# Kernel optimization log

Hardware: AMD Instinct MI355X
Metric: run time of the kernel (lower is better)

The kernel has to match this reference:

```python
import jax, jax.numpy as jnp
import numpy as np

S, B, V, E, H = 512, 16, 32003, 512, 512
HH = H // 2  # per-direction encoder hidden (bidirectional LSTM)


def _lstm(x, Wih, Whh, b, hsz):
    # x: (T, B, in); Wih: (4h, in); Whh: (4h, h); b: (4h,)  (PyTorch i,f,g,o gate order)
    xW = jnp.einsum('tbi,gi->tbg', x, Wih) + b  # precompute input projections
    h0 = jnp.zeros((x.shape[1], hsz), x.dtype)

    def step(carry, xt):
        h, c = carry
        g = xt + h @ Whh.T
        i, f, gg, o = jnp.split(g, 4, axis=-1)
        c = jax.nn.sigmoid(f) * c + jax.nn.sigmoid(i) * jnp.tanh(gg)
        h = jax.nn.sigmoid(o) * jnp.tanh(c)
        return (h, c), h

    _, hs = jax.lax.scan(step, (h0, h0), xW)
    return hs  # (T, B, hsz)


def setup_inputs() -> dict:
    key = jax.random.key(0)
    k = jax.random.split(key, 16)
    sc = 0.08
    return {
        'numeric': jax.random.randint(k[0], (S, B), 0, V, dtype=jnp.int32),
        'numeric_noised': jax.random.randint(k[1], (S, B), 0, V, dtype=jnp.int32),
        'emb': jax.random.normal(k[2], (V, E), jnp.float32) * sc,
        'enc_Wih_f': jax.random.normal(k[3], (4 * HH, E), jnp.float32) * sc,
        'enc_Whh_f': jax.random.normal(k[4], (4 * HH, HH), jnp.float32) * sc,
        'enc_b_f': jnp.zeros((4 * HH,), jnp.float32),
        'enc_Wih_b': jax.random.normal(k[5], (4 * HH, E), jnp.float32) * sc,
        'enc_Whh_b': jax.random.normal(k[6], (4 * HH, HH), jnp.float32) * sc,
        'enc_b_b': jnp.zeros((4 * HH,), jnp.float32),
        'dec_Wih': jax.random.normal(k[7], (4 * H, E), jnp.float32) * sc,
        'dec_Whh': jax.random.normal(k[8], (4 * H, H), jnp.float32) * sc,
        'dec_b': jnp.zeros((4 * H,), jnp.float32),
        'attn_W': jax.random.normal(k[9], (H, H), jnp.float32) * sc,
        'mlp_W': jax.random.normal(k[10], (H, 2 * H), jnp.float32) * sc,
        'mlp_b': jnp.zeros((H,), jnp.float32),
        'out_W': jax.random.normal(k[11], (V, H), jnp.float32) * sc,
        'out_b': jnp.zeros((V,), jnp.float32),
    }


def reference(numeric, numeric_noised, emb, enc_Wih_f, enc_Whh_f, enc_b_f,
              enc_Wih_b, enc_Whh_b, enc_b_b, dec_Wih, dec_Whh, dec_b,
              attn_W, mlp_W, mlp_b, out_W, out_b):
    zero = jnp.zeros((1, B), numeric.dtype)  # zeroBeginning (<SOS>=0)
    num = jnp.concatenate([zero, numeric], 0)            # (S+1, B)
    noised = jnp.concatenate([zero, numeric_noised], 0)  # (S+1, B)
    inp_t, tgt = num[:-1], num[1:]
    embedded = emb[inp_t]        # (S, B, E)
    emb_noised = emb[noised]     # (S+1, B, E)

    # BiLSTM encoder (hidden H/2 per direction)
    ef = _lstm(emb_noised, enc_Wih_f, enc_Whh_f, enc_b_f, HH)
    eb = _lstm(emb_noised[::-1], enc_Wih_b, enc_Whh_b, enc_b_b, HH)[::-1]
    enc = jnp.concatenate([ef, eb], -1)                  # (S+1, B, H)

    # LSTM decoder (teacher forced)
    dec = _lstm(embedded, dec_Wih, dec_Whh, dec_b, H)    # (S, B, H)

    # attention: scores over encoder positions s, softmax on dim s
    proj = jnp.einsum('sbh,kh->sbk', enc, attn_W)        # attention_proj (no bias)
    scores = jnp.einsum('sbh,tbh->bst', proj, dec)       # (B, S+1, S)
    attn = jax.nn.softmax(scores, axis=1)
    # context: equivalent of (enc.unsqueeze(2)*attn.unsqueeze(3)).sum(0).transpose(0,1)
    ctx = jnp.einsum('sbh,bst->tbh', enc, attn)          # (S, B, H)

    full = jnp.concatenate([dec, ctx], -1)               # (S, B, 2H)
    hid = jax.nn.relu(jnp.einsum('tbf,hf->tbh', full, mlp_W) + mlp_b)
    logits = jnp.einsum('tbh,vh->tbv', hid, out_W) + out_b
    logp = jax.nn.log_softmax(logits, -1)

    # NLLLoss with ignore_index=0, mean over non-ignored tokens
    nll = -jnp.take_along_axis(logp, tgt[..., None].astype(jnp.int32), axis=-1)[..., 0]
    mask = (tgt != 0).astype(logp.dtype)
    return (nll * mask).sum() / mask.sum()
```

## Files before the change

kernel.cpp:

```cpp
#include <hip/hip_runtime.h>
#include <stdint.h>
#include <stddef.h>


typedef __attribute__((ext_vector_type(8))) short  sx8;
typedef __attribute__((ext_vector_type(8))) __bf16 bfx8;
typedef __attribute__((ext_vector_type(4))) float  fx4;

#define NCHUNK 251

__device__ __forceinline__ float bf2f(short h) {
  unsigned u = ((unsigned)(unsigned short)h) << 16;
  return __builtin_bit_cast(float, u);
}
__device__ __forceinline__ short f2bf(float f) {
  unsigned u = __builtin_bit_cast(unsigned, f);
  u = (u + 0x7fffu + ((u >> 16) & 1u)) >> 16;
  return (short)u;
}
__device__ __forceinline__ fx4 mfma_bf16(sx8 a, sx8 b, fx4 c) {
  return __builtin_amdgcn_mfma_f32_16x16x32_bf16(
      __builtin_bit_cast(bfx8, a), __builtin_bit_cast(bfx8, b), c, 0, 0, 0);
}
__device__ __forceinline__ float sigm(float x) { return 1.f / (1.f + __expf(-x)); }
__device__ __forceinline__ float tanh_f(float x) { return 2.f / (1.f + __expf(-2.f * x)) - 1.f; }

__global__ void k_f32_to_bf16(const float* __restrict__ src, short* __restrict__ dst, long n) {
  long i = (long)blockIdx.x * 256 + threadIdx.x;
  long stride = (long)gridDim.x * 256;
  for (; i < n; i += stride) dst[i] = f2bf(src[i]);
}

__global__ void k_embed(const float* __restrict__ emb, const int* __restrict__ idx,
                        short* __restrict__ dst, int rows) {
  long i = (long)blockIdx.x * 256 + threadIdx.x;
  if (i >= (long)rows * 512) return;
  int r = (int)(i >> 9), c = (int)(i & 511);
  int tok = (r < 16) ? 0 : idx[r - 16];
  dst[i] = f2bf(emb[(size_t)tok * 512 + c]);
}

#define BM 128
#define BN 128
#define BK 32
__global__ __launch_bounds__(256) void k_gemm_bt(
    const short* __restrict__ A, long lda, long sA,
    const short* __restrict__ B, long ldb, long sB,
    short* __restrict__ Cb, float* __restrict__ Cf, long ldc, long sC,
    const float* __restrict__ bias, int relu,
    int M, int N, int K) {
  __shared__ short As[BM * BK];
  __shared__ short Bs[BN * BK];
  const int bz = blockIdx.z;
  const short* Ab = A + (size_t)bz * sA;
  const short* Bb = B + (size_t)bz * sB;
  const int m0 = blockIdx.x * BM, n0 = blockIdx.y * BN;
  const int tid = threadIdx.x;
  const int lane = tid & 63, wave = tid >> 6;
  const int wr = wave >> 1, wc = wave & 1;
  const int q = lane >> 4, l15 = lane & 15;
  const int sr = tid >> 2;
  const int sc = (tid & 3) * 8;

  fx4 acc[4][4] = {};

  for (int k0 = 0; k0 < K; k0 += BK) {
    __syncthreads();
    *(sx8*)&As[ sr       * BK + sc] = *(const sx8*)(Ab + (size_t)(m0 + sr)      * lda + k0 + sc);
    *(sx8*)&As[(sr + 64) * BK + sc] = *(const sx8*)(Ab + (size_t)(m0 + sr + 64) * lda + k0 + sc);
    *(sx8*)&Bs[ sr       * BK + sc] = *(const sx8*)(Bb + (size_t)(n0 + sr)      * ldb + k0 + sc);
    *(sx8*)&Bs[(sr + 64) * BK + sc] = *(const sx8*)(Bb + (size_t)(n0 + sr + 64) * ldb + k0 + sc);
    __syncthreads();
    sx8 af[4], bf[4];
#pragma unroll
    for (int i = 0; i < 4; i++) af[i] = *(const sx8*)&As[(wr * 64 + i * 16 + l15) * BK + q * 8];
#pragma unroll
    for (int j = 0; j < 4; j++) bf[j] = *(const sx8*)&Bs[(wc * 64 + j * 16 + l15) * BK + q * 8];
#pragma unroll
    for (int i = 0; i < 4; i++)
#pragma unroll
      for (int j = 0; j < 4; j++) acc[i][j] = mfma_bf16(af[i], bf[j], acc[i][j]);
  }

#pragma unroll
  for (int i = 0; i < 4; i++) {
    int row0 = m0 + wr * 64 + i * 16 + q * 4;
#pragma unroll
    for (int j = 0; j < 4; j++) {
      int col = n0 + wc * 64 + j * 16 + l15;
      if (col >= N) continue;
      float bv = bias ? bias[col] : 0.f;
#pragma unroll
      for (int r = 0; r < 4; r++) {
        int row = row0 + r;
        if (row >= M) continue;
        float v = acc[i][j][r] + bv;
        if (relu) v = fmaxf(v, 0.f);
        size_t o = (size_t)bz * sC + (size_t)row * ldc + col;
        if (Cb) Cb[o] = f2bf(v);
        else    Cf[o] = v;
      }
    }
  }
}

__global__ __launch_bounds__(256) void k_gemm_lse(
    const short* __restrict__ A, const short* __restrict__ B,
    const float* __restrict__ bias,
    float* __restrict__ mp, float* __restrict__ sp,
    int N, int K) {
  __shared__ short As[BM * BK];
  __shared__ short Bs[BN * BK];
  __shared__ float redm[2][2][64];
  __shared__ float reds[2][2][64];
  const int m0 = blockIdx.x * BM, n0 = blockIdx.y * BN;
  const int tid = threadIdx.x;
  const int lane = tid & 63, wave = tid >> 6;
  const int wr = wave >> 1, wc = wave & 1;
  const int q = lane >> 4, l15 = lane & 15;
  const int sr = tid >> 2, sc = (tid & 3) * 8;

  fx4 acc[4][4] = {};
  for (int k0 = 0; k0 < K; k0 += BK) {
    __syncthreads();
    *(sx8*)&As[ sr       * BK + sc] = *(const sx8*)(A + (size_t)(m0 + sr)      * K + k0 + sc);
    *(sx8*)&As[(sr + 64) * BK + sc] = *(const sx8*)(A + (size_t)(m0 + sr + 64) * K + k0 + sc);
    *(sx8*)&Bs[ sr       * BK + sc] = *(const sx8*)(B + (size_t)(n0 + sr)      * K + k0 + sc);
    *(sx8*)&Bs[(sr + 64) * BK + sc] = *(const sx8*)(B + (size_t)(n0 + sr + 64) * K + k0 + sc);
    __syncthreads();
    sx8 af[4], bf[4];
#pragma unroll
    for (int i = 0; i < 4; i++) af[i] = *(const sx8*)&As[(wr * 64 + i * 16 + l15) * BK + q * 8];
#pragma unroll
    for (int j = 0; j < 4; j++) bf[j] = *(const sx8*)&Bs[(wc * 64 + j * 16 + l15) * BK + q * 8];
#pragma unroll
    for (int i = 0; i < 4; i++)
#pragma unroll
      for (int j = 0; j < 4; j++) acc[i][j] = mfma_bf16(af[i], bf[j], acc[i][j]);
  }

#pragma unroll
  for (int i = 0; i < 4; i++) {
#pragma unroll
    for (int r = 0; r < 4; r++) {
      float vj[4], mx = -1e30f;
#pragma unroll
      for (int j = 0; j < 4; j++) {
        int col = n0 + wc * 64 + j * 16 + l15;
        float v = (col < N) ? (acc[i][j][r] + bias[col]) : -1e30f;
        vj[j] = v;
        mx = fmaxf(mx, v);
      }
#pragma unroll
      for (int off = 1; off < 16; off <<= 1) mx = fmaxf(mx, __shfl_xor(mx, off, 64));
      float s = 0.f;
#pragma unroll
      for (int j = 0; j < 4; j++) s += __expf(vj[j] - mx);
#pragma unroll
      for (int off = 1; off < 16; off <<= 1) s += __shfl_xor(s, off, 64);
      if (l15 == 0) {
        int rl = i * 16 + q * 4 + r;
        redm[wr][wc][rl] = mx;
        reds[wr][wc][rl] = s;
      }
    }
  }
  __syncthreads();
  if (tid < 128) {
    int wrr = tid >> 6, rl = tid & 63;
    float ma = redm[wrr][0][rl], mb = redm[wrr][1][rl];
    float M2 = fmaxf(ma, mb);
    float S2 = reds[wrr][0][rl] * __expf(ma - M2) + reds[wrr][1][rl] * __expf(mb - M2);
    int grow = m0 + wrr * 64 + rl;
    mp[(size_t)blockIdx.y * 8192 + grow] = M2;
    sp[(size_t)blockIdx.y * 8192 + grow] = S2;
  }
}

template<int NU, int NK, int HD, int T, int GRP>
__device__ __forceinline__ void lstm_body(
    const short* __restrict__ xW, const short* __restrict__ Whh,
    short* __restrict__ outb, const int ostride, const int ocol0,
    const short* __restrict__ zbuf,
    unsigned* __restrict__ flags, const int fbase, const int nw, const int gb) {
  constexpr int NT = 4 * NU;
  constexpr int N4 = 4 * HD;
  const int lane = threadIdx.x & 63, wv = threadIdx.x >> 6;
  const int q = lane >> 4, l15 = lane & 15;
  const int j0 = gb * (NU * 64) + wv * (NU * 16);
  const int slot = fbase + gb * 4 + wv;

  sx8 bfr[NT][NK];
#pragma unroll
  for (int tt = 0; tt < NT; tt++) {
    const int g = tt / NU, u = tt % NU;
    const size_t wrow = (size_t)(g * HD + j0 + u * 16 + l15);
#pragma unroll
    for (int kk = 0; kk < NK; kk++)
      bfr[tt][kk] = *(const sx8*)(Whh + wrow * HD + kk * 32 + q * 8);
  }

  float cst[NU][4] = {};
  float xg[NT][4];
  {
    const int tr0 = (GRP == 2) ? (T - 1) : 0;
#pragma unroll
    for (int tt = 0; tt < NT; tt++) {
      const int g = tt / NU, u = tt % NU;
      const int cx = g * HD + j0 + u * 16 + l15;
#pragma unroll
      for (int r = 0; r < 4; r++)
        xg[tt][r] = bf2f(xW[(size_t)(tr0 * 16 + q * 4 + r) * N4 + cx]);
    }
  }

  for (int t = 0; t < T; t++) {
    const int trow = (GRP == 2) ? (T - 1 - t) : t;

    if (t > 0) {
      const unsigned tgt = (unsigned)t;
      while (true) {
        unsigned v = tgt;
        if (lane < nw)
          v = __hip_atomic_load(&flags[(size_t)(fbase + lane) * 16],
                                __ATOMIC_RELAXED, __HIP_MEMORY_SCOPE_AGENT);
        if (__all((int)(v >= tgt))) break;
        __builtin_amdgcn_s_sleep(1);
      }
      __threadfence();
    }

    const short* hp;
    if (t == 0) hp = zbuf;
    else {
      const int prow = (GRP == 2) ? (trow + 1) : (trow - 1);
      hp = outb + (size_t)(prow * 16) * ostride + ocol0;
    }
    sx8 afr[NK];
#pragma unroll
    for (int kk = 0; kk < NK; kk++)
      afr[kk] = *(const sx8*)(hp + (size_t)l15 * ostride + kk * 32 + q * 8);

    fx4 acc[NT] = {};
#pragma unroll
    for (int kk = 0; kk < NK; kk++)
#pragma unroll
      for (int tt = 0; tt < NT; tt++)
        acc[tt] = mfma_bf16(afr[kk], bfr[tt][kk], acc[tt]);

#pragma unroll
    for (int u = 0; u < NU; u++) {
      const int col = ocol0 + j0 + u * 16 + l15;
#pragma unroll
      for (int r = 0; r < 4; r++) {
        float gi = acc[0 * NU + u][r] + xg[0 * NU + u][r];
        float gf = acc[1 * NU + u][r] + xg[1 * NU + u][r];
        float gc = acc[2 * NU + u][r] + xg[2 * NU + u][r];
        float go = acc[3 * NU + u][r] + xg[3 * NU + u][r];
        float cn = sigm(gf) * cst[u][r] + sigm(gi) * tanh_f(gc);
        cst[u][r] = cn;
        outb[(size_t)(trow * 16 + q * 4 + r) * ostride + col] = f2bf(sigm(go) * tanh_f(cn));
      }
    }

    __threadfence();
    if (lane == 0)
      __hip_atomic_store(&flags[(size_t)slot * 16], (unsigned)(t + 1),
                         __ATOMIC_RELAXED, __HIP_MEMORY_SCOPE_AGENT);

    if (t + 1 < T) {
      const int ntr = (GRP == 2) ? (T - 2 - t) : (t + 1);
#pragma unroll
      for (int tt = 0; tt < NT; tt++) {
        const int g = tt / NU, u = tt % NU;
        const int cx = g * HD + j0 + u * 16 + l15;
#pragma unroll
        for (int r = 0; r < 4; r++)
          xg[tt][r] = bf2f(xW[(size_t)(ntr * 16 + q * 4 + r) * N4 + cx]);
      }
    }
  }
}

__global__ __launch_bounds__(256, 1) void k_lstm(
    const short* __restrict__ xW_d, const short* __restrict__ Wh_d,
    const short* __restrict__ xW_f, const short* __restrict__ Wh_f,
    const short* __restrict__ xW_b, const short* __restrict__ Wh_b,
    short* __restrict__ full, short* __restrict__ enc,
    const short* __restrict__ zbuf, unsigned* __restrict__ flags) {
  const int blk = blockIdx.x;
  if (blk < 8)
    lstm_body<1, 16, 512, 512, 0>(xW_d, Wh_d, full, 1024, 0,   zbuf, flags, 0, 32, blk);
  else if (blk < 10)
    lstm_body<2, 8, 256, 513, 1>(xW_f, Wh_f, enc, 512, 0,   zbuf, flags, 32, 8, blk - 8);
  else
    lstm_body<2, 8, 256, 513, 2>(xW_b, Wh_b, enc, 512, 256, zbuf, flags, 40, 8, blk - 10);
}

__global__ void k_softmax(short* __restrict__ scores) {
  const int b = blockIdx.y;
  const int t = blockIdx.x * 256 + threadIdx.x;
  short* base = scores + (size_t)b * 513 * 512 + t;
  float mx = -1e30f;
  for (int s = 0; s < 513; s++) mx = fmaxf(mx, bf2f(base[s * 512]));
  float sum = 0.f;
  for (int s = 0; s < 513; s++) sum += __expf(bf2f(base[s * 512]) - mx);
  float inv = 1.f / sum;
  for (int s = 0; s < 513; s++) base[s * 512] = f2bf(__expf(bf2f(base[s * 512]) - mx) * inv);
}

__global__ void k_transpose(const short* __restrict__ in, long ldi, long sbi,
                            short* __restrict__ out, long ldo, long sbo,
                            int rows, int cols) {
  __shared__ short tile[32][33];
  const int bz = blockIdx.z;
  const int r0 = blockIdx.x * 32, c0 = blockIdx.y * 32;
  const int tx = threadIdx.x & 31, ty = threadIdx.x >> 5;
#pragma unroll
  for (int i = 0; i < 4; i++) {
    int r = r0 + ty + i * 8, c = c0 + tx;
    short v = 0;
    if (r < rows) v = in[(size_t)bz * sbi + (size_t)r * ldi + c];
    tile[ty + i * 8][tx] = v;
  }
  __syncthreads();
#pragma unroll
  for (int i = 0; i < 4; i++) {
    int oc = c0 + ty + i * 8, orr = r0 + tx;
    if (orr < rows) out[(size_t)bz * sbo + (size_t)oc * ldo + orr] = tile[tx][ty + i * 8];
  }
}

__global__ __launch_bounds__(256) void k_tl(const short* __restrict__ hid,
                                            const short* __restrict__ W,
                                            const float* __restrict__ ob,
                                            const int* __restrict__ tgt,
                                            float* __restrict__ tl) {
  const int row = blockIdx.x * 4 + (threadIdx.x >> 6);
  const int lane = threadIdx.x & 63;
  const int tv = tgt[row];
  sx8 hv = *(const sx8*)(hid + (size_t)row * 512 + lane * 8);
  sx8 wv = *(const sx8*)(W + (size_t)tv * 512 + lane * 8);
  float s = 0.f;
#pragma unroll
  for (int e = 0; e < 8; e++) s += bf2f(hv[e]) * bf2f(wv[e]);
#pragma unroll
  for (int off = 32; off >= 1; off >>= 1) s += __shfl_down(s, off, 64);
  if (lane == 0) tl[row] = s + ob[tv];
}

__global__ __launch_bounds__(256) void k_nll(const float* __restrict__ mp,
                                             const float* __restrict__ sp,
                                             const float* __restrict__ tl,
                                             const int* __restrict__ tgt,
                                             float* __restrict__ accum) {
  const int r = blockIdx.x * 256 + threadIdx.x;
  float M = -1e30f, Ssum = 0.f;
  for (int c = 0; c < NCHUNK; c++) {
    float m = mp[(size_t)c * 8192 + r];
    float s = sp[(size_t)c * 8192 + r];
    float nM = fmaxf(M, m);
    Ssum = Ssum * __expf(M - nM) + s * __expf(m - nM);
    M = nM;
  }
  float msk = (tgt[r] != 0) ? 1.f : 0.f;
  float nll = (M + logf(Ssum) - tl[r]) * msk;
#pragma unroll
  for (int off = 32; off >= 1; off >>= 1) {
    nll += __shfl_down(nll, off, 64);
    msk += __shfl_down(msk, off, 64);
  }
  if ((threadIdx.x & 63) == 0) {
    atomicAdd(&accum[0], nll);
    atomicAdd(&accum[1], msk);
  }
}

__global__ void k_final(const float* __restrict__ accum, float* __restrict__ out) {
  out[0] = accum[0] / accum[1];
}

extern "C" void kernel_launch(void* const* d_in, const int* in_sizes, int n_in,
                              void* d_out, int out_size, void* d_ws, size_t ws_size,
                              hipStream_t stream) {
  (void)in_sizes; (void)n_in; (void)out_size;
  const int*   numeric = (const int*)  d_in[0];
  const int*   noised  = (const int*)  d_in[1];
  const float* emb     = (const float*)d_in[2];
  const float* Wih_f   = (const float*)d_in[3];
  const float* Whh_f   = (const float*)d_in[4];
  const float* b_f     = (const float*)d_in[5];
  const float* Wih_b   = (const float*)d_in[6];
  const float* Whh_b   = (const float*)d_in[7];
  const float* b_b     = (const float*)d_in[8];
  const float* dWih    = (const float*)d_in[9];
  const float* dWhh    = (const float*)d_in[10];
  const float* d_bv    = (const float*)d_in[11];
  const float* attnW   = (const float*)d_in[12];
  const float* mlpW    = (const float*)d_in[13];
  const float* mlp_b   = (const float*)d_in[14];
  const float* outW    = (const float*)d_in[15];
  const float* out_b   = (const float*)d_in[16];
  float* out = (float*)d_out;

  char* w = (char*)d_ws;
  size_t off = 0;
  auto alloc = [&](size_t bytes) -> void* {
    void* p = w + off;
    off = (off + bytes + 255) & ~(size_t)255;
    return p;
  };
  short* bWih_f = (short*)alloc((size_t)1024 * 512 * 2);
  short* bWih_b = (short*)alloc((size_t)1024 * 512 * 2);
  short* bWhh_f = (short*)alloc((size_t)1024 * 256 * 2);
  short* bWhh_b = (short*)alloc((size_t)1024 * 256 * 2);
  short* bWdec  = (short*)alloc((size_t)2048 * 512 * 2);
  short* bWhhd  = (short*)alloc((size_t)2048 * 512 * 2);
  short* battnW = (short*)alloc((size_t)512 * 512 * 2);
  short* bmlpW  = (short*)alloc((size_t)512 * 1024 * 2);
  short* boutW  = (short*)alloc((size_t)32768 * 512 * 2);
  short* embedded  = (short*)alloc((size_t)8192 * 512 * 2);
  short* embnoised = (short*)alloc((size_t)8208 * 512 * 2);
  short* g_xwf     = (short*)alloc((size_t)8208 * 1024 * 2);
  short* g_xwb     = (short*)alloc((size_t)8208 * 1024 * 2);
  short* g_xwd     = (short*)alloc((size_t)8192 * 2048 * 2);
  short* enc       = (short*)alloc((size_t)8208 * 512 * 2);
  short* proj      = (short*)alloc((size_t)8208 * 512 * 2);
  short* scores    = (short*)alloc((size_t)16 * 513 * 512 * 2);
  short* attnT     = (short*)alloc((size_t)16 * 512 * 544 * 2);
  short* encT      = (short*)alloc((size_t)16 * 512 * 544 * 2);
  short* full      = (short*)alloc((size_t)8192 * 1024 * 2);
  short* hid       = (short*)alloc((size_t)8192 * 512 * 2);
  float* mpart     = (float*)alloc((size_t)NCHUNK * 8192 * 4);
  float* spart     = (float*)alloc((size_t)NCHUNK * 8192 * 4);
  float* tlv       = (float*)alloc((size_t)8192 * 4);
  size_t small_off = off;
  short*    zbuf  = (short*)alloc((size_t)16384 * 2);
  unsigned* flags = (unsigned*)alloc(4096);
  float*    accum = (float*)alloc(256);
  size_t total = off;
  if (ws_size < total) return;

  dim3 b256(256);

  hipMemsetAsync(boutW, 0, (size_t)32768 * 512 * 2, stream);
  hipMemsetAsync(attnT, 0, (size_t)16 * 512 * 544 * 2, stream);
  hipMemsetAsync(encT, 0, (size_t)16 * 512 * 544 * 2, stream);
  hipMemsetAsync(w + small_off, 0, total - small_off, stream);

  k_f32_to_bf16<<<2048, b256, 0, stream>>>(Wih_f, bWih_f, 1024L * 512);
  k_f32_to_bf16<<<2048, b256, 0, stream>>>(Wih_b, bWih_b, 1024L * 512);
  k_f32_to_bf16<<<2048, b256, 0, stream>>>(Whh_f, bWhh_f, 1024L * 256);
  k_f32_to_bf16<<<2048, b256, 0, stream>>>(Whh_b, bWhh_b, 1024L * 256);
  k_f32_to_bf16<<<2048, b256, 0, stream>>>(dWih,  bWdec,  2048L * 512);
  k_f32_to_bf16<<<2048, b256, 0, stream>>>(dWhh,  bWhhd,  2048L * 512);
  k_f32_to_bf16<<<2048, b256, 0, stream>>>(attnW, battnW, 512L * 512);
  k_f32_to_bf16<<<2048, b256, 0, stream>>>(mlpW,  bmlpW,  512L * 1024);
  k_f32_to_bf16<<<8192, b256, 0, stream>>>(outW,  boutW,  32003L * 512);

  k_embed<<<(8192 * 512 + 255) / 256, b256, 0, stream>>>(emb, numeric, embedded, 8192);
  k_embed<<<(8208 * 512 + 255) / 256, b256, 0, stream>>>(emb, noised, embnoised, 8208);

  k_gemm_bt<<<dim3(65, 8, 1), b256, 0, stream>>>(embnoised, 512, 0, bWih_f, 512, 0,
      g_xwf, nullptr, 1024, 0, b_f, 0, 8208, 1024, 512);
  k_gemm_bt<<<dim3(65, 8, 1), b256, 0, stream>>>(embnoised, 512, 0, bWih_b, 512, 0,
      g_xwb, nullptr, 1024, 0, b_b, 0, 8208, 1024, 512);
  k_gemm_bt<<<dim3(64, 16, 1), b256, 0, stream>>>(embedded, 512, 0, bWdec, 512, 0,
      g_xwd, nullptr, 2048, 0, d_bv, 0, 8192, 2048, 512);

  k_lstm<<<12, b256, 0, stream>>>(g_xwd, bWhhd, g_xwf, bWhh_f, g_xwb, bWhh_b,
                                  full, enc, zbuf, flags);

  k_gemm_bt<<<dim3(65, 4, 1), b256, 0, stream>>>(enc, 512, 0, battnW, 512, 0,
      proj, nullptr, 512, 0, nullptr, 0, 8208, 512, 512);

  k_gemm_bt<<<dim3(5, 4, 16), b256, 0, stream>>>(proj, 8192, 512, full, 16384, 1024,
      scores, nullptr, 512, (long)513 * 512, nullptr, 0, 513, 512, 512);

  k_softmax<<<dim3(2, 16), b256, 0, stream>>>(scores);

  k_transpose<<<dim3(17, 16, 16), b256, 0, stream>>>(scores, 512, (long)513 * 512,
      attnT, 544, (long)512 * 544, 513, 512);
  k_transpose<<<dim3(17, 16, 16), b256, 0, stream>>>(enc, 8192, 512,
      encT, 544, (long)512 * 544, 513, 512);

  k_gemm_bt<<<dim3(4, 4, 16), b256, 0, stream>>>(attnT, 544, (long)512 * 544,
      encT, 544, (long)512 * 544,
      full + 512, nullptr, 16384, 1024, nullptr, 0, 512, 512, 544);

  k_gemm_bt<<<dim3(64, 4, 1), b256, 0, stream>>>(full, 1024, 0, bmlpW, 1024, 0,
      hid, nullptr, 512, 0, mlp_b, 1, 8192, 512, 1024);

  k_gemm_lse<<<dim3(64, NCHUNK), b256, 0, stream>>>(hid, boutW, out_b, mpart, spart,
                                                    32003, 512);
  k_tl<<<2048, b256, 0, stream>>>(hid, boutW, out_b, numeric, tlv);
  k_nll<<<32, b256, 0, stream>>>(mpart, spart, tlv, numeric, accum);
  k_final<<<1, 1, 0, stream>>>(accum, out);
}
```

Measured before the change: 5.504 ms.

## Replace per-wave flags and fences with per-block flags and atomic h loads

Reworks the cross-block step synchronisation in the persistent LSTM kernel. Each block now publishes one flag after a __syncthreads, instead of every wave setting its own padded flag after a __threadfence. The polling waves check fewer flags without sleeping, and the hidden state is read and written through relaxed agent-scope atomics instead of relying on fences. Outputs are packed two bf16 per dword via a lane shuffle so the atomic stores stay aligned. This is meant to cut the latency of the serial per-timestep barrier, but relaxed atomics without fences or acquire ordering weaken the memory-ordering guarantees, and the flags are no longer padded apart.

```diff
diff --git a/kernel.cpp b/kernel.cpp
--- a/kernel.cpp
+++ b/kernel.cpp
@@ -24,6 +24,17 @@
 }
 __device__ __forceinline__ float sigm(float x) { return 1.f / (1.f + __expf(-x)); }
 __device__ __forceinline__ float tanh_f(float x) { return 2.f / (1.f + __expf(-2.f * x)) - 1.f; }
+
+__device__ __forceinline__ unsigned long long cp_load_u64(const void* p) {
+  return __hip_atomic_load((const unsigned long long*)p,
+                           __ATOMIC_RELAXED, __HIP_MEMORY_SCOPE_AGENT);
+}
+__device__ __forceinline__ sx8 cp_load_sx8(const void* p) {
+  union { unsigned long long u[2]; sx8 v; } cvt;
+  cvt.u[0] = cp_load_u64(p);
+  cvt.u[1] = cp_load_u64((const char*)p + 8);
+  return cvt.v;
+}
 
 __global__ void k_f32_to_bf16(const float* __restrict__ src, short* __restrict__ dst, long n) {
   long i = (long)blockIdx.x * 256 + threadIdx.x;
@@ -182,13 +193,12 @@
     const short* __restrict__ xW, const short* __restrict__ Whh,
     short* __restrict__ outb, const int ostride, const int ocol0,
     const short* __restrict__ zbuf,
-    unsigned* __restrict__ flags, const int fbase, const int nw, const int gb) {
+    unsigned* __restrict__ flags, const int fbase, const int nb, const int gb) {
   constexpr int NT = 4 * NU;
   constexpr int N4 = 4 * HD;
   const int lane = threadIdx.x & 63, wv = threadIdx.x >> 6;
   const int q = lane >> 4, l15 = lane & 15;
   const int j0 = gb * (NU * 64) + wv * (NU * 16);
-  const int slot = fbase + gb * 4 + wv;
 
   sx8 bfr[NT][NK];
 #pragma unroll
@@ -221,13 +231,11 @@
       const unsigned tgt = (unsigned)t;
       while (true) {
         unsigned v = tgt;
-        if (lane < nw)
-          v = __hip_atomic_load(&flags[(size_t)(fbase + lane) * 16],
+        if (lane < nb)
+          v = __hip_atomic_load(&flags[fbase + lane],
                                 __ATOMIC_RELAXED, __HIP_MEMORY_SCOPE_AGENT);
         if (__all((int)(v >= tgt))) break;
-        __builtin_amdgcn_s_sleep(1);
       }
-      __threadfence();
     }
 
     const short* hp;
@@ -239,7 +247,7 @@
     sx8 afr[NK];
 #pragma unroll
     for (int kk = 0; kk < NK; kk++)
-      afr[kk] = *(const sx8*)(hp + (size_t)l15 * ostride + kk * 32 + q * 8);
+      afr[kk] = cp_load_sx8(hp + (size_t)l15 * ostride + kk * 32 + q * 8);
 
     fx4 acc[NT] = {};
 #pragma unroll
@@ -250,7 +258,7 @@
 
 #pragma unroll
     for (int u = 0; u < NU; u++) {
-      const int col = ocol0 + j0 + u * 16 + l15;
+      const int colb = ocol0 + j0 + u * 16 + (l15 & ~1);
 #pragma unroll
       for (int r = 0; r < 4; r++) {
         float gi = acc[0 * NU + u][r] + xg[0 * NU + u][r];
@@ -259,13 +267,19 @@
         float go = acc[3 * NU + u][r] + xg[3 * NU + u][r];
         float cn = sigm(gf) * cst[u][r] + sigm(gi) * tanh_f(gc);
         cst[u][r] = cn;
-        outb[(size_t)(trow * 16 + q * 4 + r) * ostride + col] = f2bf(sigm(go) * tanh_f(cn));
+        unsigned mine = (unsigned)(unsigned short)f2bf(sigm(go) * tanh_f(cn));
+        unsigned other = (unsigned)__shfl_xor((int)mine, 1, 64);
+        if (!(l15 & 1)) {
+          unsigned dw = mine | (other << 16);
+          unsigned* dst = (unsigned*)(outb + (size_t)(trow * 16 + q * 4 + r) * ostride + colb);
+          __hip_atomic_store(dst, dw, __ATOMIC_RELAXED, __HIP_MEMORY_SCOPE_AGENT);
+        }
       }
     }
 
-    __threadfence();
-    if (lane == 0)
-      __hip_atomic_store(&flags[(size_t)slot * 16], (unsigned)(t + 1),
+    __syncthreads();
+    if (threadIdx.x == 0)
+      __hip_atomic_store(&flags[fbase + gb], (unsigned)(t + 1),
                          __ATOMIC_RELAXED, __HIP_MEMORY_SCOPE_AGENT);
 
     if (t + 1 < T) {
@@ -290,11 +304,11 @@
     const short* __restrict__ zbuf, unsigned* __restrict__ flags) {
   const int blk = blockIdx.x;
   if (blk < 8)
-    lstm_body<1, 16, 512, 512, 0>(xW_d, Wh_d, full, 1024, 0,   zbuf, flags, 0, 32, blk);
+    lstm_body<1, 16, 512, 512, 0>(xW_d, Wh_d, full, 1024, 0,   zbuf, flags, 0, 8, blk);
   else if (blk < 10)
-    lstm_body<2, 8, 256, 513, 1>(xW_f, Wh_f, enc, 512, 0,   zbuf, flags, 32, 8, blk - 8);
+    lstm_body<2, 8, 256, 513, 1>(xW_f, Wh_f, enc, 512, 0,   zbuf, flags, 32, 2, blk - 8);
   else
-    lstm_body<2, 8, 256, 513, 2>(xW_b, Wh_b, enc, 512, 256, zbuf, flags, 40, 8, blk - 10);
+    lstm_body<2, 8, 256, 513, 2>(xW_b, Wh_b, enc, 512, 256, zbuf, flags, 64, 2, blk - 10);
 }
 
 __global__ void k_softmax(short* __restrict__ scores) {
```

Measured after the change: 4.428 ms. 1.24x faster.
